# Kernel optimization log

Measured on AMD Instinct MI355X. Metric: run time of the kernel, lower is better.

## Reference

```python
import jax, jax.numpy as jnp
import numpy as np

NEG_INF = -1e9


def setup_inputs() -> dict:
    key = jax.random.key(0)
    k1, k2, k3, k4, k5, k6 = jax.random.split(key, 6)
    B, P, N, C, H = 32, 512, 64, 9, 128
    polylines = jax.random.normal(k1, (B, P, N, C), dtype=jnp.float32)
    polylines_mask = jax.random.uniform(k2, (B, P, N)) > 0.1
    # MLP params (Linear(C,H) -> ReLU -> Linear(H,H)), torch-style init scale
    W1 = jax.random.uniform(k3, (C, H), minval=-1.0, maxval=1.0) / jnp.sqrt(C)
    b1 = jax.random.uniform(k4, (H,), minval=-1.0, maxval=1.0) / jnp.sqrt(C)
    W2 = jax.random.uniform(k5, (H, H), minval=-1.0, maxval=1.0) / jnp.sqrt(H)
    b2 = jax.random.uniform(k6, (H,), minval=-1.0, maxval=1.0) / jnp.sqrt(H)
    return {"polylines": polylines, "polylines_mask": polylines_mask,
            "W1": W1, "b1": b1, "W2": W2, "b2": b2}


def reference(polylines, polylines_mask, W1, b1, W2, b2):
    # Point MLP applied to all points (invalid ones are overwritten below,
    # identical math to the torch masked-gather version).
    h = jax.nn.relu(jnp.einsum('bpnc,ch->bpnh', polylines, W1) + b1)
    feat = jnp.einsum('bpnh,hd->bpnd', h, W2) + b2  # [B,P,N,H]
    feat = jnp.where(polylines_mask[..., None], feat, NEG_INF)
    pooled = jnp.max(feat, axis=2)  # [B,P,H]
    # Polylines with no valid points pooled to NEG_INF -> zero them out.
    any_valid = jnp.any(polylines_mask, axis=2)  # [B,P]
    return jnp.where(any_valid[..., None], pooled, 0.0)
```

## Files before the change

### kernel.cpp

```cpp
#include <hip/hip_runtime.h>


using bf16x8 = __attribute__((ext_vector_type(8))) short;
using f32x4  = __attribute__((ext_vector_type(4))) float;

#define MFMA32(A,B,C) __builtin_amdgcn_mfma_f32_16x16x32_bf16((A),(B),(C),0,0,0)

__device__ __forceinline__ f32x4 vmax4(f32x4 a, f32x4 b) {
  return __builtin_elementwise_max(a, b);
}

__device__ __forceinline__ unsigned short f2bf(float f) {
  union { float f; unsigned int u; } v; v.f = f;
  unsigned int r = v.u + 0x7fffu + ((v.u >> 16) & 1u);
  return (unsigned short)(r >> 16);
}

__device__ __forceinline__ unsigned int pk2(float a, float b) {
  unsigned int r;
  asm("v_cvt_pk_bf16_f32 %0, %1, %2" : "=v"(r) : "v"(a), "v"(b));
  return r;
}

__global__ void prep1(const float* __restrict__ W1, const float* __restrict__ W2,
                      const void* __restrict__ mask,
                      unsigned short* __restrict__ w1sw, unsigned short* __restrict__ w2sw,
                      int* __restrict__ flag) {
  int b = blockIdx.x, t = threadIdx.x;
  if (b == 0) {
    __shared__ int cnt;
    if (t == 0) cnt = 0;
    __syncthreads();
    const unsigned char* mb = (const unsigned char*)mask;
    int local = 0;
    for (int i = t * 16; i < t * 16 + 16; i++) local += (mb[i] != 0) ? 1 : 0;
    atomicAdd(&cnt, local);
    __syncthreads();
    if (t == 0) *flag = (cnt > 2800) ? 1 : 0;
  } else if (b <= 2) {
    int e = (b - 1) * 256 + t;
    int lane = e & 63, grp = e >> 6;
    int li = lane & 15, q = lane >> 4;
    int h = grp * 16 + li;
    int c0 = q * 8;
    #pragma unroll
    for (int j = 0; j < 8; j++) {
      int c = c0 + j;
      w1sw[e * 8 + j] = f2bf((c < 9) ? W1[c * 128 + h] : 0.f);
    }
  } else {
    int e = (b - 3) * 256 + t;
    if (e < 2048) {
      int lane = e & 63, grp = e >> 6;
      int wr = grp >> 4, sub = grp & 15;
      int ks = sub >> 2, td = sub & 3;
      int li = lane & 15, q = lane >> 4;
      int d = wr * 64 + td * 16 + li;
      int h0 = ks * 32 + q * 8;
      #pragma unroll
      for (int j = 0; j < 8; j++)
        w2sw[e * 8 + j] = f2bf(W2[(h0 + j) * 128 + d]);
    }
  }
}

__global__ __launch_bounds__(128, 4) void poly_main_k(
    const float* __restrict__ X, const void* __restrict__ mask,
    const float* __restrict__ b1g, const float* __restrict__ b2g,
    const unsigned short* __restrict__ w1sw, const unsigned short* __restrict__ w2sw,
    const int* __restrict__ flagp, float* __restrict__ out)
{
  __shared__ __align__(16) unsigned char smem[18688];
  unsigned short* Hb = (unsigned short*)smem;
  float*          P  = (float*)smem;
  float*          Xs = (float*)(smem + 16384);

  const int tid  = threadIdx.x;
  const int lane = tid & 63;
  const int wr   = tid >> 6;
  const int li   = lane & 15, q = lane >> 4;

  {
    const char* xg = (const char*)X + (long long)blockIdx.x * 2304;
    unsigned ldsoff = (unsigned)(tid & 64) * 16;
    __builtin_amdgcn_global_load_lds(
        (const __attribute__((address_space(1))) unsigned int*)(xg + tid * 16),
        (__attribute__((address_space(3))) unsigned int*)((char*)Xs + ldsoff),
        16, 0, 0);
    if (tid < 16)
      __builtin_amdgcn_global_load_lds(
          (const __attribute__((address_space(1))) unsigned int*)(xg + 2048 + tid * 16),
          (__attribute__((address_space(3))) unsigned int*)((char*)Xs + 2048),
          16, 0, 0);
  }

  float mf[4];
  {
    int flag = *flagp;
    long long mb = (long long)blockIdx.x * 64 + li;
    if (flag) {
      const unsigned char* mp = (const unsigned char*)mask;
      #pragma unroll
      for (int tm = 0; tm < 4; tm++) mf[tm] = mp[mb + tm * 16] ? 0.f : -4e9f;
    } else {
      const int* mp = (const int*)mask;
      #pragma unroll
      for (int tm = 0; tm < 4; tm++) mf[tm] = mp[mb + tm * 16] ? 0.f : -4e9f;
    }
  }

  __syncthreads();

  bf16x8 bx[4];
  #pragma unroll
  for (int tm = 0; tm < 4; tm++) {
    const float* xr = Xs + (tm * 16 + li) * 9;
    union { bf16x8 v; unsigned int u[4]; } uu;
    uu.u[0] = uu.u[1] = uu.u[2] = uu.u[3] = 0u;
    if (q == 0) {
      uu.u[0] = pk2(xr[0], xr[1]); uu.u[1] = pk2(xr[2], xr[3]);
      uu.u[2] = pk2(xr[4], xr[5]); uu.u[3] = pk2(xr[6], xr[7]);
    } else if (q == 1) {
      uu.u[0] = pk2(xr[8], 0.f);
    }
    bx[tm] = uu.v;
  }

  #pragma unroll
  for (int th = 0; th < 4; th++) {
    bf16x8 a1 = *(const bf16x8*)(w1sw + ((wr * 4 + th) * 64 + lane) * 8);
    f32x4 bv = *(const f32x4*)(b1g + wr * 64 + th * 16 + q * 4);
    f32x4 acc[4];
    #pragma unroll
    for (int tm = 0; tm < 4; tm++) acc[tm] = bv;
    __builtin_amdgcn_s_setprio(1);
    #pragma unroll
    for (int tm = 0; tm < 4; tm++) acc[tm] = MFMA32(a1, bx[tm], acc[tm]);
    __builtin_amdgcn_s_setprio(0);
    #pragma unroll
    for (int tm = 0; tm < 4; tm++) {
      int m = tm * 16 + li;
      f32x4 v = vmax4(acc[tm], f32x4{0.f, 0.f, 0.f, 0.f});
      uint2 hv;
      hv.x = pk2(v[0], v[1]);
      hv.y = pk2(v[2], v[3]);
      int chunk = (wr * 8 + th * 2 + (q >> 1)) ^ li;
      *(uint2*)(Hb + m * 128 + chunk * 8 + (q & 1) * 4) = hv;
    }
  }
  __syncthreads();

  f32x4 pooled[4];
  #pragma unroll
  for (int tm = 0; tm < 4; tm++) {
    int m = tm * 16 + li;
    f32x4 acc[4];
    #pragma unroll
    for (int td = 0; td < 4; td++) acc[td] = f32x4{0.f, 0.f, 0.f, 0.f};
    #pragma unroll
    for (int ks = 0; ks < 4; ks++) {
      int chunk = (ks * 4 + q) ^ li;
      bf16x8 bb = *(const bf16x8*)(Hb + m * 128 + chunk * 8);
      __builtin_amdgcn_s_setprio(1);
      #pragma unroll
      for (int td = 0; td < 4; td++) {
        bf16x8 a2 = *(const bf16x8*)(w2sw + (((wr * 16 + ks * 4 + td) * 64) + lane) * 8);
        acc[td] = MFMA32(a2, bb, acc[td]);
      }
      __builtin_amdgcn_s_setprio(0);
    }
    if (tm == 0) {
      #pragma unroll
      for (int td = 0; td < 4; td++) pooled[td] = acc[td] + mf[0];
    } else {
      #pragma unroll
      for (int td = 0; td < 4; td++) pooled[td] = vmax4(pooled[td], acc[td] + mf[tm]);
    }
  }
  #pragma unroll
  for (int td = 0; td < 4; td++)
    pooled[td] += *(const f32x4*)(b2g + wr * 64 + td * 16 + q * 4);

  __syncthreads();
  #pragma unroll
  for (int td = 0; td < 4; td++)
    *(f32x4*)(P + li * 132 + wr * 64 + td * 16 + q * 4) = pooled[td];
  __syncthreads();

  {
    const float* Pp = P + tid;
    float v = Pp[0];
    #pragma unroll
    for (int j = 1; j < 16; j++) v = fmaxf(v, Pp[j * 132]);
    if (v < -1e8f) v = 0.f;
    out[(long long)blockIdx.x * 128 + tid] = v;
  }
}

extern "C" void kernel_launch(void* const* d_in, const int* in_sizes, int n_in,
                              void* d_out, int out_size, void* d_ws, size_t ws_size,
                              hipStream_t stream) {
  const float* X    = (const float*)d_in[0];
  const void*  mask = d_in[1];
  const float* W1   = (const float*)d_in[2];
  const float* b1   = (const float*)d_in[3];
  const float* W2   = (const float*)d_in[4];
  const float* b2   = (const float*)d_in[5];
  float* out = (float*)d_out;

  unsigned short* w1sw = (unsigned short*)d_ws;
  unsigned short* w2sw = (unsigned short*)((char*)d_ws + 8192);
  int* flag            = (int*)((char*)d_ws + 40960);

  prep1<<<11, 256, 0, stream>>>(W1, W2, mask, w1sw, w2sw, flag);
  poly_main_k<<<16384, 128, 0, stream>>>(X, mask, b1, b2, w1sw, w2sw, flag, out);
}
```

Baseline: 161.2 us.

## Process two polylines per block and reduce pooled max with warp shuffles

Each block now handles two polylines using four waves, with each wave pair covering one polyline. The final max-pool over points is done with xor shuffles across the 16-lane group instead of an LDS transpose plus two barriers, and the s_setprio hints around the MFMAs are removed. The aim is to halve the block count, drop the shared-memory reduction stage, and amortise per-block overhead. In exchange the kernel doubles its LDS use per block, which may lower occupancy, and adds shuffle instructions.

New measurement: 145.5 us. -9.7%, faster.

```diff
diff --git a/kernel.cpp b/kernel.cpp
--- a/kernel.cpp
+++ b/kernel.cpp
@@ -19,6 +19,15 @@
 __device__ __forceinline__ unsigned int pk2(float a, float b) {
   unsigned int r;
   asm("v_cvt_pk_bf16_f32 %0, %1, %2" : "=v"(r) : "v"(a), "v"(b));
+  return r;
+}
+
+__device__ __forceinline__ f32x4 shfl_xor4(f32x4 v, int m) {
+  f32x4 r;
+  r[0] = __shfl_xor(v[0], m);
+  r[1] = __shfl_xor(v[1], m);
+  r[2] = __shfl_xor(v[2], m);
+  r[3] = __shfl_xor(v[3], m);
   return r;
 }
 
@@ -64,40 +73,39 @@
   }
 }
 
-__global__ __launch_bounds__(128, 4) void poly_main_k(
+__global__ __launch_bounds__(256, 4) void poly_main_k(
     const float* __restrict__ X, const void* __restrict__ mask,
     const float* __restrict__ b1g, const float* __restrict__ b2g,
     const unsigned short* __restrict__ w1sw, const unsigned short* __restrict__ w2sw,
     const int* __restrict__ flagp, float* __restrict__ out)
 {
-  __shared__ __align__(16) unsigned char smem[18688];
+  __shared__ __align__(16) unsigned char smem[37376];
   unsigned short* Hb = (unsigned short*)smem;
-  float*          P  = (float*)smem;
-  float*          Xs = (float*)(smem + 16384);
+  float*          Xs = (float*)(smem + 32768);
 
   const int tid  = threadIdx.x;
   const int lane = tid & 63;
-  const int wr   = tid >> 6;
+  const int w    = tid >> 6;
+  const int wr   = w >> 1, wc = w & 1;
   const int li   = lane & 15, q = lane >> 4;
 
   {
-    const char* xg = (const char*)X + (long long)blockIdx.x * 2304;
-    unsigned ldsoff = (unsigned)(tid & 64) * 16;
+    const char* xg = (const char*)X + (long long)blockIdx.x * 4608;
     __builtin_amdgcn_global_load_lds(
         (const __attribute__((address_space(1))) unsigned int*)(xg + tid * 16),
-        (__attribute__((address_space(3))) unsigned int*)((char*)Xs + ldsoff),
+        (__attribute__((address_space(3))) unsigned int*)((char*)Xs + w * 1024),
         16, 0, 0);
-    if (tid < 16)
+    if (tid < 32)
       __builtin_amdgcn_global_load_lds(
-          (const __attribute__((address_space(1))) unsigned int*)(xg + 2048 + tid * 16),
-          (__attribute__((address_space(3))) unsigned int*)((char*)Xs + 2048),
+          (const __attribute__((address_space(1))) unsigned int*)(xg + 4096 + tid * 16),
+          (__attribute__((address_space(3))) unsigned int*)((char*)Xs + 4096),
           16, 0, 0);
   }
 
   float mf[4];
   {
     int flag = *flagp;
-    long long mb = (long long)blockIdx.x * 64 + li;
+    long long mb = (long long)blockIdx.x * 128 + wc * 64 + li;
     if (flag) {
       const unsigned char* mp = (const unsigned char*)mask;
       #pragma unroll
@@ -114,7 +122,8 @@
   bf16x8 bx[4];
   #pragma unroll
   for (int tm = 0; tm < 4; tm++) {
-    const float* xr = Xs + (tm * 16 + li) * 9;
+    int m = wc * 64 + tm * 16 + li;
+    const float* xr = Xs + m * 9;
     union { bf16x8 v; unsigned int u[4]; } uu;
     uu.u[0] = uu.u[1] = uu.u[2] = uu.u[3] = 0u;
     if (q == 0) {
@@ -133,13 +142,11 @@
     f32x4 acc[4];
     #pragma unroll
     for (int tm = 0; tm < 4; tm++) acc[tm] = bv;
-    __builtin_amdgcn_s_setprio(1);
     #pragma unroll
     for (int tm = 0; tm < 4; tm++) acc[tm] = MFMA32(a1, bx[tm], acc[tm]);
-    __builtin_amdgcn_s_setprio(0);
     #pragma unroll
     for (int tm = 0; tm < 4; tm++) {
-      int m = tm * 16 + li;
+      int m = wc * 64 + tm * 16 + li;
       f32x4 v = vmax4(acc[tm], f32x4{0.f, 0.f, 0.f, 0.f});
       uint2 hv;
       hv.x = pk2(v[0], v[1]);
@@ -153,7 +160,7 @@
   f32x4 pooled[4];
   #pragma unroll
   for (int tm = 0; tm < 4; tm++) {
-    int m = tm * 16 + li;
+    int m = wc * 64 + tm * 16 + li;
     f32x4 acc[4];
     #pragma unroll
     for (int td = 0; td < 4; td++) acc[td] = f32x4{0.f, 0.f, 0.f, 0.f};
@@ -161,13 +168,11 @@
     for (int ks = 0; ks < 4; ks++) {
       int chunk = (ks * 4 + q) ^ li;
       bf16x8 bb = *(const bf16x8*)(Hb + m * 128 + chunk * 8);
-      __builtin_amdgcn_s_setprio(1);
       #pragma unroll
       for (int td = 0; td < 4; td++) {
         bf16x8 a2 = *(const bf16x8*)(w2sw + (((wr * 16 + ks * 4 + td) * 64) + lane) * 8);
         acc[td] = MFMA32(a2, bb, acc[td]);
       }
-      __builtin_amdgcn_s_setprio(0);
     }
     if (tm == 0) {
       #pragma unroll
@@ -177,23 +182,23 @@
       for (int td = 0; td < 4; td++) pooled[td] = vmax4(pooled[td], acc[td] + mf[tm]);
     }
   }
-  #pragma unroll
-  for (int td = 0; td < 4; td++)
-    pooled[td] += *(const f32x4*)(b2g + wr * 64 + td * 16 + q * 4);
-
-  __syncthreads();
-  #pragma unroll
-  for (int td = 0; td < 4; td++)
-    *(f32x4*)(P + li * 132 + wr * 64 + td * 16 + q * 4) = pooled[td];
-  __syncthreads();
-
-  {
-    const float* Pp = P + tid;
-    float v = Pp[0];
-    #pragma unroll
-    for (int j = 1; j < 16; j++) v = fmaxf(v, Pp[j * 132]);
-    if (v < -1e8f) v = 0.f;
-    out[(long long)blockIdx.x * 128 + tid] = v;
+
+  #pragma unroll
+  for (int td = 0; td < 4; td++) {
+    #pragma unroll
+    for (int sm = 1; sm < 16; sm <<= 1)
+      pooled[td] = vmax4(pooled[td], shfl_xor4(pooled[td], sm));
+  }
+
+  if (li == 0) {
+    float* op = out + (long long)blockIdx.x * 256 + wc * 128 + wr * 64 + q * 4;
+    #pragma unroll
+    for (int td = 0; td < 4; td++) {
+      f32x4 v = pooled[td] + *(const f32x4*)(b2g + wr * 64 + td * 16 + q * 4);
+      #pragma unroll
+      for (int j = 0; j < 4; j++) if (v[j] < -1e8f) v[j] = 0.f;
+      *(f32x4*)(op + td * 16) = v;
+    }
   }
 }
 
@@ -213,5 +218,5 @@
   int* flag            = (int*)((char*)d_ws + 40960);
 
   prep1<<<11, 256, 0, stream>>>(W1, W2, mask, w1sw, w2sw, flag);
-  poly_main_k<<<16384, 128, 0, stream>>>(X, mask, b1, b2, w1sw, w2sw, flag, out);
-}
+  poly_main_k<<<8192, 256, 0, stream>>>(X, mask, b1, b2, w1sw, w2sw, flag, out);
+}
```
